# Kernel optimization log

Measured on AMD Instinct MI355X. Metric: run time of the kernel, lower is better.

## Reference

```python
import jax, jax.numpy as jnp
import numpy as np

B = 4        # pair batch
V = 2        # num_views
C = 256      # channels
NH = 4       # num_heads
H = 128
W = 128
G = 8        # GroupNorm groups
EPS = 1e-5


def setup_inputs() -> dict:
    key = jax.random.key(0)
    ks = jax.random.split(key, 5)
    x = jax.random.normal(ks[0], (B * V, C, H, W), jnp.float32)
    gn_gamma = jnp.ones((C,), jnp.float32)
    gn_beta = jnp.zeros((C,), jnp.float32)
    w_qkv = jax.random.normal(ks[1], (3 * C, C), jnp.float32) * 0.02
    b_qkv = jax.random.normal(ks[2], (3 * C,), jnp.float32) * 0.02
    w_proj = jax.random.normal(ks[3], (C, C), jnp.float32) * 0.02
    b_proj = jax.random.normal(ks[4], (C,), jnp.float32) * 0.02
    return {"x": x, "gn_gamma": gn_gamma, "gn_beta": gn_beta,
            "w_qkv": w_qkv, "b_qkv": b_qkv, "w_proj": w_proj, "b_proj": b_proj}


def reference(x, gn_gamma, gn_beta, w_qkv, b_qkv, w_proj, b_proj):
    bv, c, h, w = x.shape
    v, nh = V, NH
    hd = c // nh
    b = bv // v
    scale = hd ** -0.5

    # GroupNorm(8, c): normalize over (c/G, h, w) per group, biased variance
    xg = x.reshape(bv, G, c // G, h, w)
    mean = xg.mean(axis=(2, 3, 4), keepdims=True)
    var = xg.var(axis=(2, 3, 4), keepdims=True)
    xn = ((xg - mean) * jax.lax.rsqrt(var + EPS)).reshape(bv, c, h, w)
    xn = xn * gn_gamma[:, None, None] + gn_beta[:, None, None]

    # 1x1 conv qkv: (bv, 3c, h, w)
    qkv = jnp.einsum('oc,bchw->bohw', w_qkv, xn) + b_qkv[:, None, None]

    # '(b v) (three nh hd) h w -> three b nh (h w) v hd'
    qkv = qkv.reshape(b, v, 3, nh, hd, h * w).transpose(2, 0, 3, 5, 1, 4)
    q, k, val = qkv[0], qkv[1], qkv[2]  # each (b, nh, hw, v, hd)

    # tiny VxV attention per pixel
    attn = jax.nn.softmax(jnp.einsum('bnpvd,bnpud->bnpvu', q, k) * scale, axis=-1)
    out = jnp.einsum('bnpvu,bnpud->bnpvd', attn, val)  # (b, nh, hw, v, hd)

    # 'b nh (h w) v hd -> (b v) (nh hd) h w'
    out = out.transpose(0, 3, 1, 4, 2).reshape(bv, c, h, w)

    # proj 1x1 conv + residual
    out = jnp.einsum('oc,bchw->bohw', w_proj, out) + b_proj[:, None, None]
    return x + out
```

## Files before the change

### kernel.cpp

```cpp
#include <hip/hip_runtime.h>
#include <stdint.h>

#define HW 16384
#define CCH 256
#define NROWS 131072
#define GROUP_ELEMS 524288
#define BK 64
#define LDSP 72

typedef __attribute__((ext_vector_type(8))) short bfrag8;
typedef __attribute__((ext_vector_type(8))) unsigned short us8;
typedef __attribute__((ext_vector_type(4))) float facc4;

static __device__ __forceinline__ unsigned short f2b(float f) {
  union { float f; unsigned int u; } x; x.f = f;
  unsigned int r = x.u + 0x7FFFu + ((x.u >> 16) & 1u);
  return (unsigned short)(r >> 16);
}
static __device__ __forceinline__ float b2f(unsigned short h) {
  union { float f; unsigned int u; } x; x.u = ((unsigned int)h) << 16;
  return x.f;
}

static __device__ __forceinline__ void gload_lds16(const unsigned short* g, unsigned short* l) {
  __builtin_amdgcn_global_load_lds(
      (const __attribute__((address_space(1))) unsigned int*)g,
      (__attribute__((address_space(3))) unsigned int*)l, 16, 0, 0);
}

__global__ void k_red(const float* __restrict__ x, float* __restrict__ red) {
  int gg = blockIdx.x >> 3, sp = blockIdx.x & 7;
  const float4* p = (const float4*)(x + (size_t)gg * GROUP_ELEMS + (size_t)sp * 65536);
  float s = 0.f, ss = 0.f;
  for (int i = 0; i < 64; ++i) {
    float4 v = p[i * 256 + threadIdx.x];
    s  += v.x + v.y + v.z + v.w;
    ss += v.x*v.x + v.y*v.y + v.z*v.z + v.w*v.w;
  }
  for (int off = 32; off; off >>= 1) { s += __shfl_xor(s, off); ss += __shfl_xor(ss, off); }
  __shared__ float ls[4], lss[4];
  int w = threadIdx.x >> 6;
  if ((threadIdx.x & 63) == 0) { ls[w] = s; lss[w] = ss; }
  __syncthreads();
  if (threadIdx.x == 0) {
    float S = ls[0]+ls[1]+ls[2]+ls[3], SS = lss[0]+lss[1]+lss[2]+lss[3];
    atomicAdd(&red[gg*2], S); atomicAdd(&red[gg*2+1], SS);
  }
}

__global__ void k_fin(const float* __restrict__ red, float* __restrict__ stats) {
  int g = threadIdx.x;
  float s = red[g*2], ss = red[g*2+1];
  float mean = s / (float)GROUP_ELEMS;
  float var = ss / (float)GROUP_ELEMS - mean*mean;
  stats[g*2] = mean;
  stats[g*2+1] = rsqrtf(var + 1e-5f);
}

__global__ void k_cast(const float* __restrict__ wq, const float* __restrict__ wp,
                       unsigned short* __restrict__ wqb, unsigned short* __restrict__ wpb) {
  int i = blockIdx.x * 256 + threadIdx.x;
  if (i < 768*256) {
    int h = i / 49152;
    int rem = i % 49152;
    int kk = rem / 6144;
    int rem2 = rem % 6144;
    int j = rem2 >> 9;
    int lane = (rem2 >> 3) & 63;
    int e = rem2 & 7;
    int q4 = lane >> 4, lm = lane & 15;
    int cl = j*16 + lm;
    int part = cl >> 6, d = cl & 63;
    int o = part*256 + h*64 + d;
    int k = kk*32 + q4*8 + e;
    wqb[i] = f2b(wq[o*256 + k]);
  } else {
    int j = i - 768*256;
    wpb[j] = f2b(wp[j]);
  }
}

__global__ void k_norm_t(const float* __restrict__ x, const float* __restrict__ stats,
                         const float* __restrict__ gamma, const float* __restrict__ beta,
                         unsigned short* __restrict__ xnt) {
  __shared__ float tile[64][65];
  int bx = blockIdx.x;
  int bv = bx >> 10;
  int rem = bx & 1023;
  int p0 = (rem >> 2) * 64, c0 = (rem & 3) * 64;
  int pair = bv >> 1, v = bv & 1;
  int t = threadIdx.x;
  int p_off = t & 63, c4 = t >> 6;
  const float* xsrc = x + (size_t)bv * CCH * HW;
  for (int cc = 0; cc < 16; ++cc) {
    int c_loc = c4 * 16 + cc;
    int c = c0 + c_loc;
    float val = xsrc[(size_t)c * HW + p0 + p_off];
    int g = bv * 8 + (c >> 5);
    float xn = (val - stats[g*2]) * stats[g*2+1] * gamma[c] + beta[c];
    tile[p_off][c_loc] = xn;
  }
  __syncthreads();
  for (int it = 0; it < 8; ++it) {
    int u = it * 256 + t;
    int p = u >> 5, c2 = u & 31;
    int c = c0 + c2*2;
    unsigned int pk = (unsigned int)f2b(tile[p][c2*2]) | ((unsigned int)f2b(tile[p][c2*2+1]) << 16);
    int P = p0 + p;
    int n = pair*2048 + (P >> 3);
    int s = (P & 7) + 8*v;
    size_t addr = (size_t)n*4096 + (size_t)(c >> 5)*512 + (size_t)((c & 31) >> 3)*128
                + (size_t)s*8 + (c & 7);
    *(unsigned int*)(xnt + addr) = pk;
  }
}

__global__ __launch_bounds__(256, 2) void k_qkv_attn(
    const unsigned short* __restrict__ A,
    const unsigned short* __restrict__ B,
    const float* __restrict__ bq,
    unsigned short* __restrict__ attn_out) {
  __shared__ __align__(16) unsigned short Blds[24 * 512];
  int h = blockIdx.x;
  int row0 = blockIdx.y * 128;
  int t = threadIdx.x;
  int w = t >> 6, lane = t & 63;
  int lm = lane & 15, q4 = lane >> 4;

  size_t aBase = (size_t)((row0 + w*32) >> 4) * 4096 + (size_t)lane * 8;
  const unsigned short* Bh = B + (size_t)h * 49152;

  facc4 acc[2][12];
  #pragma unroll
  for (int j = 0; j < 12; ++j) {
    facc4 bb = *(const facc4*)(bq + (j >> 2)*256 + h*64 + (j & 3)*16 + q4*4);
    acc[0][j] = bb; acc[1][j] = bb;
  }

  #pragma unroll
  for (int c = 0; c < 4; ++c) {
    #pragma unroll
    for (int i = 0; i < 6; ++i) {
      int f = w*6 + i;
      gload_lds16(Bh + (size_t)(c*24 + f)*512 + (size_t)lane*8, &Blds[f*512]);
    }
    bfrag8 a[2][2];
    #pragma unroll
    for (int kk2 = 0; kk2 < 2; ++kk2)
      #pragma unroll
      for (int p = 0; p < 2; ++p)
        a[kk2][p] = *(const bfrag8*)(A + aBase + (size_t)p*4096 + (size_t)(c*2 + kk2)*512);
    __syncthreads();
    #pragma unroll
    for (int kk2 = 0; kk2 < 2; ++kk2) {
      #pragma unroll
      for (int j = 0; j < 12; ++j) {
        bfrag8 wf = *(const bfrag8*)(&Blds[(kk2*12 + j)*512 + lane*8]);
        acc[0][j] = __builtin_amdgcn_mfma_f32_16x16x32_bf16(wf, a[kk2][0], acc[0][j], 0, 0, 0);
        acc[1][j] = __builtin_amdgcn_mfma_f32_16x16x32_bf16(wf, a[kk2][1], acc[1][j], 0, 0, 0);
      }
    }
    __syncthreads();
  }

  #pragma unroll
  for (int i = 0; i < 2; ++i) {
    float s_same = 0.f, s_cross = 0.f;
    #pragma unroll
    for (int jj = 0; jj < 4; ++jj) {
      #pragma unroll
      for (int r = 0; r < 4; ++r) {
        float qv = acc[i][jj][r];
        float kv = acc[i][4 + jj][r];
        float kx = __shfl_xor(kv, 8);
        s_same  += qv * kv;
        s_cross += qv * kx;
      }
    }
    s_same  += __shfl_xor(s_same, 16);  s_same  += __shfl_xor(s_same, 32);
    s_cross += __shfl_xor(s_cross, 16); s_cross += __shfl_xor(s_cross, 32);
    float s0 = s_same * 0.125f, s1 = s_cross * 0.125f;
    float m = fmaxf(s0, s1);
    float e0 = __expf(s0 - m), e1 = __expf(s1 - m);
    float inv = 1.f / (e0 + e1);
    float w_self = e0 * inv, w_cross = e1 * inv;

    int rg = row0 + w*32 + i*16;
    int pg = (rg >> 1) + (lm & 7);
    int v = lm >> 3;
    int pair = pg >> 14, p = pg & 16383;
    unsigned short* dst = attn_out + ((size_t)((pair*2 + v)*16384 + p))*256 + h*64 + q4*4;
    #pragma unroll
    for (int jj = 0; jj < 4; ++jj) {
      float o[4];
      #pragma unroll
      for (int r = 0; r < 4; ++r) {
        float vv = acc[i][8 + jj][r];
        float vx = __shfl_xor(vv, 8);
        o[r] = w_self * vv + w_cross * vx;
      }
      uint2 pk;
      pk.x = (unsigned int)f2b(o[0]) | ((unsigned int)f2b(o[1]) << 16);
      pk.y = (unsigned int)f2b(o[2]) | ((unsigned int)f2b(o[3]) << 16);
      *(uint2*)(dst + jj*16) = pk;
    }
  }
}

__global__ __launch_bounds__(256, 2) void k_gemm_proj(
    const unsigned short* __restrict__ A,
    const unsigned short* __restrict__ B,
    const float* __restrict__ bias,
    const float* __restrict__ x,
    float* __restrict__ out) {
  __shared__ unsigned short As[128][LDSP];
  __shared__ unsigned short Bs[128][LDSP];
  int col0 = blockIdx.x * 128;
  int row0 = blockIdx.y * 128;
  int t = threadIdx.x;
  int w = t >> 6, lane = t & 63;
  int wm = w & 1, wn = w >> 1;
  int lm = lane & 15, q = lane >> 4;
  facc4 acc[4][4] = {};
  for (int kc = 0; kc < 4; ++kc) {
    for (int i = 0; i < 4; ++i) {
      int flat = i * 256 + t;
      int r = flat >> 3, g = flat & 7;
      *(us8*)(&As[r][g*8]) = *(const us8*)(A + (size_t)(row0 + r)*256 + kc*BK + g*8);
      *(us8*)(&Bs[r][g*8]) = *(const us8*)(B + (size_t)(col0 + r)*256 + kc*BK + g*8);
    }
    __syncthreads();
    for (int ks = 0; ks < 2; ++ks) {
      bfrag8 a[4], b[4];
      for (int i = 0; i < 4; ++i) a[i] = *(const bfrag8*)(&As[wm*64 + i*16 + lm][ks*32 + q*8]);
      for (int j = 0; j < 4; ++j) b[j] = *(const bfrag8*)(&Bs[wn*64 + j*16 + lm][ks*32 + q*8]);
      for (int i = 0; i < 4; ++i)
        for (int j = 0; j < 4; ++j)
          acc[i][j] = __builtin_amdgcn_mfma_f32_16x16x32_bf16(a[i], b[j], acc[i][j], 0, 0, 0);
    }
    __syncthreads();
  }
  for (int i = 0; i < 4; ++i) {
    for (int r = 0; r < 4; ++r) {
      int o = row0 + wm*64 + i*16 + q*4 + r;
      float bi = bias[o];
      for (int j = 0; j < 4; ++j) {
        int n = col0 + wn*64 + j*16 + lm;
        int bv = n >> 14, p = n & 16383;
        size_t gidx = ((size_t)bv * 256 + o) * 16384 + p;
        out[gidx] = acc[i][j][r] + bi + x[gidx];
      }
    }
  }
}

extern "C" void kernel_launch(void* const* d_in, const int* in_sizes, int n_in,
                              void* d_out, int out_size, void* d_ws, size_t ws_size,
                              hipStream_t stream) {
  const float* x     = (const float*)d_in[0];
  const float* gamma = (const float*)d_in[1];
  const float* beta  = (const float*)d_in[2];
  const float* wq    = (const float*)d_in[3];
  const float* bq    = (const float*)d_in[4];
  const float* wp    = (const float*)d_in[5];
  const float* bp    = (const float*)d_in[6];
  float* out = (float*)d_out;

  char* ws = (char*)d_ws;
  float* red   = (float*)ws;
  float* stats = (float*)(ws + 512);
  unsigned short* wqb = (unsigned short*)(ws + 1024);
  unsigned short* wpb = (unsigned short*)(ws + 1024 + 393216);
  size_t off = 1024 + 393216 + 131072;
  unsigned short* xnt = (unsigned short*)(ws + off); off += (size_t)NROWS * 256 * 2;
  unsigned short* att = (unsigned short*)(ws + off);

  hipMemsetAsync(red, 0, 1024, stream);
  k_cast<<<1024, 256, 0, stream>>>(wq, wp, wqb, wpb);
  k_red<<<512, 256, 0, stream>>>(x, red);
  k_fin<<<1, 64, 0, stream>>>(red, stats);
  k_norm_t<<<8192, 256, 0, stream>>>(x, stats, gamma, beta, xnt);
  k_qkv_attn<<<dim3(4, 1024), 256, 0, stream>>>(xnt, wqb, bq, att);
  k_gemm_proj<<<dim3(1024, 2), 256, 0, stream>>>(wpb, att, bp, x, out);
}
```

Measured before the change: 411.6 us.

## Store attention output in MFMA fragment layout and restructure proj GEMM

The attention kernel now writes its bf16 output directly in a pre-swizzled MFMA fragment order, and the projection weights are cast into a matching fragment layout. The proj GEMM keeps the 128-row weight slab in LDS via global_load_lds, streams B fragments straight from global memory without staging, and initializes accumulators with the bias. This removes LDS staging and the syncs per K chunk for the activation operand. The trade-off is a different output store pattern and more registers per thread.

```diff
diff --git a/kernel.cpp b/kernel.cpp
--- a/kernel.cpp
+++ b/kernel.cpp
@@ -5,8 +5,6 @@
 #define CCH 256
 #define NROWS 131072
 #define GROUP_ELEMS 524288
-#define BK 64
-#define LDSP 72
 
 typedef __attribute__((ext_vector_type(8))) short bfrag8;
 typedef __attribute__((ext_vector_type(8))) unsigned short us8;
@@ -75,8 +73,16 @@
     int k = kk*32 + q4*8 + e;
     wqb[i] = f2b(wq[o*256 + k]);
   } else {
-    int j = i - 768*256;
-    wpb[j] = f2b(wp[j]);
+    int j2 = i - 768*256;
+    int rb = j2 >> 15;
+    int rem = j2 & 32767;
+    int jj = rem >> 12;
+    int kk = (rem >> 9) & 7;
+    int lane = (rem >> 3) & 63;
+    int e = rem & 7;
+    int o = rb*128 + jj*16 + (lane & 15);
+    int k = kk*32 + (lane >> 4)*8 + e;
+    wpb[j2] = f2b(wp[o*256 + k]);
   }
 }
 
@@ -186,10 +192,7 @@
     float w_self = e0 * inv, w_cross = e1 * inv;
 
     int rg = row0 + w*32 + i*16;
-    int pg = (rg >> 1) + (lm & 7);
-    int v = lm >> 3;
-    int pair = pg >> 14, p = pg & 16383;
-    unsigned short* dst = attn_out + ((size_t)((pair*2 + v)*16384 + p))*256 + h*64 + q4*4;
+    int np = rg >> 4;
     #pragma unroll
     for (int jj = 0; jj < 4; ++jj) {
       float o[4];
@@ -202,53 +205,67 @@
       uint2 pk;
       pk.x = (unsigned int)f2b(o[0]) | ((unsigned int)f2b(o[1]) << 16);
       pk.y = (unsigned int)f2b(o[2]) | ((unsigned int)f2b(o[3]) << 16);
-      *(uint2*)(dst + jj*16) = pk;
+      size_t adst = (size_t)np*4096 + (size_t)(h*2 + (jj>>1))*512
+                  + (size_t)((jj&1)*2 + (q4>>1))*128 + (size_t)lm*8 + (size_t)(q4&1)*4;
+      *(uint2*)(attn_out + adst) = pk;
     }
   }
 }
 
 __global__ __launch_bounds__(256, 2) void k_gemm_proj(
-    const unsigned short* __restrict__ A,
-    const unsigned short* __restrict__ B,
+    const unsigned short* __restrict__ Wf,
+    const unsigned short* __restrict__ Batt,
     const float* __restrict__ bias,
     const float* __restrict__ x,
     float* __restrict__ out) {
-  __shared__ unsigned short As[128][LDSP];
-  __shared__ unsigned short Bs[128][LDSP];
-  int col0 = blockIdx.x * 128;
-  int row0 = blockIdx.y * 128;
+  __shared__ __align__(16) unsigned short Wlds[64 * 512];
+  int cb = blockIdx.x;
+  int rb = blockIdx.y;
+  int row0 = rb * 128;
   int t = threadIdx.x;
   int w = t >> 6, lane = t & 63;
-  int wm = w & 1, wn = w >> 1;
-  int lm = lane & 15, q = lane >> 4;
-  facc4 acc[4][4] = {};
-  for (int kc = 0; kc < 4; ++kc) {
-    for (int i = 0; i < 4; ++i) {
-      int flat = i * 256 + t;
-      int r = flat >> 3, g = flat & 7;
-      *(us8*)(&As[r][g*8]) = *(const us8*)(A + (size_t)(row0 + r)*256 + kc*BK + g*8);
-      *(us8*)(&Bs[r][g*8]) = *(const us8*)(B + (size_t)(col0 + r)*256 + kc*BK + g*8);
-    }
-    __syncthreads();
-    for (int ks = 0; ks < 2; ++ks) {
-      bfrag8 a[4], b[4];
-      for (int i = 0; i < 4; ++i) a[i] = *(const bfrag8*)(&As[wm*64 + i*16 + lm][ks*32 + q*8]);
-      for (int j = 0; j < 4; ++j) b[j] = *(const bfrag8*)(&Bs[wn*64 + j*16 + lm][ks*32 + q*8]);
-      for (int i = 0; i < 4; ++i)
-        for (int j = 0; j < 4; ++j)
-          acc[i][j] = __builtin_amdgcn_mfma_f32_16x16x32_bf16(a[i], b[j], acc[i][j], 0, 0, 0);
-    }
-    __syncthreads();
-  }
-  for (int i = 0; i < 4; ++i) {
-    for (int r = 0; r < 4; ++r) {
-      int o = row0 + wm*64 + i*16 + q*4 + r;
-      float bi = bias[o];
-      for (int j = 0; j < 4; ++j) {
-        int n = col0 + wn*64 + j*16 + lm;
-        int bv = n >> 14, p = n & 16383;
-        size_t gidx = ((size_t)bv * 256 + o) * 16384 + p;
-        out[gidx] = acc[i][j][r] + bi + x[gidx];
+  int lm = lane & 15, q4 = lane >> 4;
+  int np0 = cb*8 + w*2;
+
+  #pragma unroll
+  for (int i = 0; i < 16; ++i) {
+    int f = w*16 + i;
+    gload_lds16(Wf + (size_t)rb*32768 + (size_t)f*512 + (size_t)lane*8, &Wlds[f*512]);
+  }
+
+  facc4 acc[2][8];
+  #pragma unroll
+  for (int j = 0; j < 8; ++j) {
+    facc4 bb = *(const facc4*)(bias + row0 + j*16 + q4*4);
+    acc[0][j] = bb; acc[1][j] = bb;
+  }
+  __syncthreads();
+
+  #pragma unroll
+  for (int kk = 0; kk < 8; ++kk) {
+    bfrag8 b0 = *(const bfrag8*)(Batt + (size_t)(np0    )*4096 + (size_t)kk*512 + (size_t)lane*8);
+    bfrag8 b1 = *(const bfrag8*)(Batt + (size_t)(np0 + 1)*4096 + (size_t)kk*512 + (size_t)lane*8);
+    #pragma unroll
+    for (int j = 0; j < 8; ++j) {
+      bfrag8 wf = *(const bfrag8*)(&Wlds[(j*8 + kk)*512 + lane*8]);
+      acc[0][j] = __builtin_amdgcn_mfma_f32_16x16x32_bf16(wf, b0, acc[0][j], 0, 0, 0);
+      acc[1][j] = __builtin_amdgcn_mfma_f32_16x16x32_bf16(wf, b1, acc[1][j], 0, 0, 0);
+    }
+  }
+
+  #pragma unroll
+  for (int p = 0; p < 2; ++p) {
+    int Rl = (np0 + p)*16 + 2*(lm & 7) + (lm >> 3);
+    int pair = Rl >> 15, remv = Rl & 32767;
+    int px = remv >> 1, v = remv & 1;
+    size_t base = ((size_t)(pair*2 + v) * 256) * 16384 + px;
+    #pragma unroll
+    for (int j = 0; j < 8; ++j) {
+      int o0 = row0 + j*16 + q4*4;
+      #pragma unroll
+      for (int r = 0; r < 4; ++r) {
+        size_t gidx = base + (size_t)(o0 + r) * 16384;
+        out[gidx] = acc[p][j][r] + x[gidx];
       }
     }
   }
```

After: 430.7 us. 1.05x slower.
